# Optimization experiments

Measured on AMD Instinct MI355X. Metric: run time of the kernel, lower is better.

## Reference

```python
import jax, jax.numpy as jnp
import numpy as np

B, S, I, H = 8, 4096, 512, 512


def setup_inputs() -> dict:
    key = jax.random.key(0)
    ks = jax.random.split(key, 5)
    s_ih = 1.0 / np.sqrt(H)
    return {
        "x": jax.random.normal(ks[0], (B, S, I), dtype=jnp.float32),
        "W_ih": jax.random.uniform(ks[1], (H, I), jnp.float32, -s_ih, s_ih),
        "W_hh": jax.random.uniform(ks[2], (H, H), jnp.float32, -s_ih, s_ih),
        "b_ih": jax.random.uniform(ks[3], (H,), jnp.float32, -s_ih, s_ih),
        "b_hh": jax.random.uniform(ks[4], (H,), jnp.float32, -s_ih, s_ih),
    }


def reference(x, W_ih, W_hh, b_ih, b_hh):
    # Precompute input contribution for all timesteps in one batched GEMM:
    # xp[b,s,h] = x[b,s,:] @ W_ih^T + b_ih
    xp = jnp.einsum("bsi,hi->bsh", x, W_ih) + b_ih  # [B,S,H]
    h0 = jnp.zeros((x.shape[0], W_hh.shape[0]), dtype=x.dtype)

    def step(h, xp_t):
        h = jnp.tanh(xp_t + h @ W_hh.T + b_hh)
        return h, h

    # scan over time (sequential recurrence)
    _, outs = jax.lax.scan(step, h0, jnp.swapaxes(xp, 0, 1))  # outs: [S,B,H]
    return jnp.swapaxes(outs, 0, 1)  # [B,S,H]
```

## Files before the change

### kernel.cpp

```cpp
#include <hip/hip_runtime.h>
#include <hip/hip_fp16.h>

#define BB 8
#define SS 4096
#define II 512
#define HH 512

typedef _Float16 h2_t __attribute__((ext_vector_type(2)));

__device__ __forceinline__ unsigned int pack_h2(float a, float b) {
    h2_t p;
    p.x = (_Float16)a;
    p.y = (_Float16)b;
    return __builtin_bit_cast(unsigned int, p);
}

__device__ __forceinline__ float dot2acc(unsigned int hp, unsigned int wp, float acc) {
#if __has_builtin(__builtin_amdgcn_fdot2)
    return __builtin_amdgcn_fdot2(__builtin_bit_cast(h2_t, hp),
                                  __builtin_bit_cast(h2_t, wp), acc, false);
#else
    h2_t h = __builtin_bit_cast(h2_t, hp);
    h2_t w = __builtin_bit_cast(h2_t, wp);
    acc = fmaf((float)h.x, (float)w.x, acc);
    acc = fmaf((float)h.y, (float)w.y, acc);
    return acc;
#endif
}

__device__ __forceinline__ float tanh_fast(float x) {
    float ax = fabsf(x);
    float t  = exp2f(-2.8853900817779268f * ax);
    float r  = (1.0f - t) * __builtin_amdgcn_rcpf(1.0f + t);
    return copysignf(r, x);
}

#define P1_TM 64
#define P1_TN 64
#define P1_TK 16
#define P1_LDP 68

__global__ __launch_bounds__(256) void xp_gemm(const float* __restrict__ x,
                                               const float* __restrict__ wih,
                                               const float* __restrict__ bih,
                                               float* __restrict__ out) {
    __shared__ float As[P1_TK][P1_LDP];
    __shared__ float Bs[P1_TK][P1_LDP];
    const int tid = threadIdx.x;
    const int n0  = blockIdx.x * P1_TN;
    const int m0  = blockIdx.y * P1_TM;
    const int row = tid >> 2;
    const int f4  = tid & 3;
    const int ty  = tid >> 4;
    const int tx  = tid & 15;

    float acc[4][4];
#pragma unroll
    for (int r = 0; r < 4; ++r)
#pragma unroll
        for (int c = 0; c < 4; ++c) acc[r][c] = 0.0f;

    const float* xa = x   + (size_t)(m0 + row) * II + f4 * 4;
    const float* wb = wih + (size_t)(n0 + row) * II + f4 * 4;

    for (int kb = 0; kb < II; kb += P1_TK) {
        float4 av = *(const float4*)(xa + kb);
        float4 bv = *(const float4*)(wb + kb);
        __syncthreads();
        As[f4 * 4 + 0][row] = av.x; As[f4 * 4 + 1][row] = av.y;
        As[f4 * 4 + 2][row] = av.z; As[f4 * 4 + 3][row] = av.w;
        Bs[f4 * 4 + 0][row] = bv.x; Bs[f4 * 4 + 1][row] = bv.y;
        Bs[f4 * 4 + 2][row] = bv.z; Bs[f4 * 4 + 3][row] = bv.w;
        __syncthreads();
#pragma unroll
        for (int kk = 0; kk < P1_TK; ++kk) {
            const float* a4 = &As[kk][ty * 4];
            const float* b4 = &Bs[kk][tx * 4];
#pragma unroll
            for (int r = 0; r < 4; ++r)
#pragma unroll
                for (int c = 0; c < 4; ++c)
                    acc[r][c] = fmaf(a4[r], b4[c], acc[r][c]);
        }
    }

    const float4 bias = *(const float4*)&bih[n0 + tx * 4];
#pragma unroll
    for (int r = 0; r < 4; ++r) {
        float4 v;
        v.x = acc[r][0] + bias.x;
        v.y = acc[r][1] + bias.y;
        v.z = acc[r][2] + bias.z;
        v.w = acc[r][3] + bias.w;
        *(float4*)(out + (size_t)(m0 + ty * 4 + r) * HH + n0 + tx * 4) = v;
    }
}

#define KREG 384
#define NREG (KREG / 2)
#define KLDS (HH - KREG)
#define W2P  66
#define LDS_DW (256 + HH * W2P)

__global__ __launch_bounds__(512, 2) void rnn_scan(const float* __restrict__ whh,
                                                   const float* __restrict__ bhh,
                                                   float* __restrict__ io) {
    extern __shared__ unsigned int lds[];
    unsigned int* hbuf = lds;
    unsigned int* w2   = lds + 256;

    const int b = blockIdx.x;
    const int j = threadIdx.x;

    unsigned int wreg[NREG];
    const float* wrow = whh + (size_t)j * HH;
#pragma unroll
    for (int q4 = 0; q4 < KREG / 4; ++q4) {
        float4 f = *(const float4*)(wrow + q4 * 4);
        wreg[2 * q4 + 0] = pack_h2(f.x, f.y);
        wreg[2 * q4 + 1] = pack_h2(f.z, f.w);
    }

    for (int idx = j; idx < HH * (KLDS / 2); idx += 512) {
        int jj = idx >> 6;
        int q  = idx & 63;
        const float* p = whh + (size_t)jj * HH + KREG + 2 * q;
        w2[jj * W2P + q] = pack_h2(p[0], p[1]);
    }
    if (j < 256) hbuf[j] = 0u;
    const float bj = bhh[j];
    __syncthreads();

    float* iob = io + (size_t)b * SS * HH;
    float xp_cur = iob[j];
    const unsigned int* wl = w2 + j * W2P;

#pragma unroll 1
    for (int t = 0; t < SS; ++t) {
        const int tn = (t + 1 < SS) ? t + 1 : t;
        float xp_next = iob[(size_t)tn * HH + j];

        float a0 = xp_cur + bj, a1 = 0.0f, a2 = 0.0f, a3 = 0.0f;

#pragma unroll
        for (int c = 0; c < NREG / 4; ++c) {
            uint4 hv = *(const uint4*)&hbuf[4 * c];
            a0 = dot2acc(hv.x, wreg[4 * c + 0], a0);
            a1 = dot2acc(hv.y, wreg[4 * c + 1], a1);
            a2 = dot2acc(hv.z, wreg[4 * c + 2], a2);
            a3 = dot2acc(hv.w, wreg[4 * c + 3], a3);
        }
#pragma unroll
        for (int c = 0; c < (KLDS / 2) / 4; ++c) {
            uint4 hv = *(const uint4*)&hbuf[NREG + 4 * c];
            uint2 wa = *(const uint2*)&wl[4 * c];
            uint2 wc = *(const uint2*)&wl[4 * c + 2];
            a0 = dot2acc(hv.x, wa.x, a0);
            a1 = dot2acc(hv.y, wa.y, a1);
            a2 = dot2acc(hv.z, wc.x, a2);
            a3 = dot2acc(hv.w, wc.y, a3);
        }

        float hnew = tanh_fast((a0 + a1) + (a2 + a3));
        iob[(size_t)t * HH + j] = hnew;
        __syncthreads();
        ((_Float16*)hbuf)[j] = (_Float16)hnew;
        __syncthreads();
        xp_cur = xp_next;
    }
}

extern "C" void kernel_launch(void* const* d_in, const int* in_sizes, int n_in,
                              void* d_out, int out_size, void* d_ws, size_t ws_size,
                              hipStream_t stream) {
    const float* x   = (const float*)d_in[0];
    const float* wih = (const float*)d_in[1];
    const float* whh = (const float*)d_in[2];
    const float* bih = (const float*)d_in[3];
    const float* bhh = (const float*)d_in[4];
    float* out = (float*)d_out;

    dim3 g1(HH / P1_TN, (BB * SS) / P1_TM);
    xp_gemm<<<g1, 256, 0, stream>>>(x, wih, bih, out);

    static_assert(LDS_DW * 4 <= 163840, "LDS over 160 KiB");
    hipFuncSetAttribute((const void*)rnn_scan,
                        hipFuncAttributeMaxDynamicSharedMemorySize, LDS_DW * 4);
    rnn_scan<<<dim3(BB), dim3(512), LDS_DW * 4, stream>>>(whh, bhh, out);
}
```

Baseline: 6.765 ms.

## Run RNN recurrence with MFMA across two cooperating blocks exchanging hidden state

Replaces the per-batch scan (one block per batch, dot2 per thread) with two blocks that each own half of the hidden columns for all 8 batches. Each block keeps its W_hh slice in registers as f16 and uses 16x16x32 MFMA on the batch-padded hidden state. After each step the blocks swap their new hidden halves through a global double-buffered mailbox, synchronised by an atomic flag spin. This removes the redundant per-batch weight traffic and turns the matvec into matrix cores, at the cost of a cross-CU global handshake every timestep and wasted MFMA rows from padding 8 batches to 16.

```diff
diff --git a/kernel.cpp b/kernel.cpp
--- a/kernel.cpp
+++ b/kernel.cpp
@@ -6,27 +6,8 @@
 #define II 512
 #define HH 512
 
-typedef _Float16 h2_t __attribute__((ext_vector_type(2)));
-
-__device__ __forceinline__ unsigned int pack_h2(float a, float b) {
-    h2_t p;
-    p.x = (_Float16)a;
-    p.y = (_Float16)b;
-    return __builtin_bit_cast(unsigned int, p);
-}
-
-__device__ __forceinline__ float dot2acc(unsigned int hp, unsigned int wp, float acc) {
-#if __has_builtin(__builtin_amdgcn_fdot2)
-    return __builtin_amdgcn_fdot2(__builtin_bit_cast(h2_t, hp),
-                                  __builtin_bit_cast(h2_t, wp), acc, false);
-#else
-    h2_t h = __builtin_bit_cast(h2_t, hp);
-    h2_t w = __builtin_bit_cast(h2_t, wp);
-    acc = fmaf((float)h.x, (float)w.x, acc);
-    acc = fmaf((float)h.y, (float)w.y, acc);
-    return acc;
-#endif
-}
+typedef _Float16 f16x8 __attribute__((ext_vector_type(8)));
+typedef float f32x4 __attribute__((ext_vector_type(4)));
 
 __device__ __forceinline__ float tanh_fast(float x) {
     float ax = fabsf(x);
@@ -96,77 +77,119 @@
     }
 }
 
-#define KREG 384
-#define NREG (KREG / 2)
-#define KLDS (HH - KREG)
-#define W2P  66
-#define LDS_DW (256 + HH * W2P)
-
-__global__ __launch_bounds__(512, 2) void rnn_scan(const float* __restrict__ whh,
-                                                   const float* __restrict__ bhh,
-                                                   float* __restrict__ io) {
-    extern __shared__ unsigned int lds[];
-    unsigned int* hbuf = lds;
-    unsigned int* w2   = lds + 256;
-
-    const int b = blockIdx.x;
-    const int j = threadIdx.x;
-
-    unsigned int wreg[NREG];
-    const float* wrow = whh + (size_t)j * HH;
-#pragma unroll
-    for (int q4 = 0; q4 < KREG / 4; ++q4) {
-        float4 f = *(const float4*)(wrow + q4 * 4);
-        wreg[2 * q4 + 0] = pack_h2(f.x, f.y);
-        wreg[2 * q4 + 1] = pack_h2(f.z, f.w);
-    }
-
-    for (int idx = j; idx < HH * (KLDS / 2); idx += 512) {
-        int jj = idx >> 6;
-        int q  = idx & 63;
-        const float* p = whh + (size_t)jj * HH + KREG + 2 * q;
-        w2[jj * W2P + q] = pack_h2(p[0], p[1]);
-    }
-    if (j < 256) hbuf[j] = 0u;
-    const float bj = bhh[j];
-    __syncthreads();
-
-    float* iob = io + (size_t)b * SS * HH;
-    float xp_cur = iob[j];
-    const unsigned int* wl = w2 + j * W2P;
-
-#pragma unroll 1
+__global__ __launch_bounds__(256, 1) void rnn_scan2(
+    const float* __restrict__ whh, const float* __restrict__ bhh,
+    float* __restrict__ io, unsigned int* __restrict__ flags,
+    uint4* __restrict__ mail ) {
+    const int bid = blockIdx.x;
+    if (bid != 0 && bid != 8) return;
+    const int p   = bid ? 1 : 0;
+    const int tid = threadIdx.x;
+    const int w   = tid >> 6;
+    const int l   = tid & 63;
+    const int l15 = l & 15;
+    const int lh  = l >> 4;
+
+    __shared__ _Float16 hh[8][264];
+
+    int ncol[4];
+#pragma unroll
+    for (int i = 0; i < 4; ++i) ncol[i] = p * 256 + (w * 4 + i) * 16 + l15;
+
+    f16x8 wf[4][16];
+#pragma unroll
+    for (int i = 0; i < 4; ++i) {
+        const float* wr = whh + (size_t)ncol[i] * HH;
+#pragma unroll
+        for (int kb = 0; kb < 16; ++kb) {
+            const int k0 = kb * 32 + lh * 8;
+            float4 x0 = *(const float4*)(wr + k0);
+            float4 x1 = *(const float4*)(wr + k0 + 4);
+            f16x8 f;
+            f[0] = (_Float16)x0.x; f[1] = (_Float16)x0.y;
+            f[2] = (_Float16)x0.z; f[3] = (_Float16)x0.w;
+            f[4] = (_Float16)x1.x; f[5] = (_Float16)x1.y;
+            f[6] = (_Float16)x1.z; f[7] = (_Float16)x1.w;
+            wf[i][kb] = f;
+        }
+    }
+    float bv[4];
+#pragma unroll
+    for (int i = 0; i < 4; ++i) bv[i] = bhh[ncol[i]];
+
     for (int t = 0; t < SS; ++t) {
-        const int tn = (t + 1 < SS) ? t + 1 : t;
-        float xp_next = iob[(size_t)tn * HH + j];
-
-        float a0 = xp_cur + bj, a1 = 0.0f, a2 = 0.0f, a3 = 0.0f;
-
-#pragma unroll
-        for (int c = 0; c < NREG / 4; ++c) {
-            uint4 hv = *(const uint4*)&hbuf[4 * c];
-            a0 = dot2acc(hv.x, wreg[4 * c + 0], a0);
-            a1 = dot2acc(hv.y, wreg[4 * c + 1], a1);
-            a2 = dot2acc(hv.z, wreg[4 * c + 2], a2);
-            a3 = dot2acc(hv.w, wreg[4 * c + 3], a3);
-        }
-#pragma unroll
-        for (int c = 0; c < (KLDS / 2) / 4; ++c) {
-            uint4 hv = *(const uint4*)&hbuf[NREG + 4 * c];
-            uint2 wa = *(const uint2*)&wl[4 * c];
-            uint2 wc = *(const uint2*)&wl[4 * c + 2];
-            a0 = dot2acc(hv.x, wa.x, a0);
-            a1 = dot2acc(hv.y, wa.y, a1);
-            a2 = dot2acc(hv.z, wc.x, a2);
-            a3 = dot2acc(hv.w, wc.y, a3);
-        }
-
-        float hnew = tanh_fast((a0 + a1) + (a2 + a3));
-        iob[(size_t)t * HH + j] = hnew;
-        __syncthreads();
-        ((_Float16*)hbuf)[j] = (_Float16)hnew;
-        __syncthreads();
-        xp_cur = xp_next;
+        float xq[4][4];
+        if (lh < 2) {
+#pragma unroll
+            for (int r = 0; r < 4; ++r) {
+                const int m = lh * 4 + r;
+                const float* row = io + ((size_t)m * SS + t) * HH;
+#pragma unroll
+                for (int i = 0; i < 4; ++i) xq[r][i] = row[ncol[i]];
+            }
+        }
+
+        f32x4 acc[4];
+#pragma unroll
+        for (int i = 0; i < 4; ++i) acc[i] = (f32x4){0.f, 0.f, 0.f, 0.f};
+
+        if (t > 0) {
+            if (tid == 0) {
+                while (__hip_atomic_load(flags + (1 - p) * 64, __ATOMIC_RELAXED,
+                                         __HIP_MEMORY_SCOPE_AGENT) < (unsigned)t)
+                    __builtin_amdgcn_s_sleep(1);
+            }
+            __syncthreads();
+            __threadfence();
+
+            const uint4* mb = mail + (size_t)((t - 1) & 1) * 1024;
+            f16x8 af[16];
+#pragma unroll
+            for (int kb = 0; kb < 16; ++kb) {
+                uint4 u = mb[kb * 64 + l];
+                af[kb] = __builtin_bit_cast(f16x8, u);
+            }
+#pragma unroll
+            for (int kb = 0; kb < 16; ++kb)
+#pragma unroll
+                for (int i = 0; i < 4; ++i)
+                    acc[i] = __builtin_amdgcn_mfma_f32_16x16x32_f16(
+                        af[kb], wf[i][kb], acc[i], 0, 0, 0);
+        }
+
+        if (lh < 2) {
+#pragma unroll
+            for (int r = 0; r < 4; ++r) {
+                const int m = lh * 4 + r;
+                float* row = io + ((size_t)m * SS + t) * HH;
+#pragma unroll
+                for (int i = 0; i < 4; ++i) {
+                    float v = tanh_fast(acc[i][r] + xq[r][i] + bv[i]);
+                    row[ncol[i]] = v;
+                    hh[m][(w * 4 + i) * 16 + l15] = (_Float16)v;
+                }
+            }
+        }
+        __syncthreads();
+
+#pragma unroll
+        for (int e2 = 0; e2 < 2; ++e2) {
+            const int e   = tid * 2 + e2;
+            const int kbl = e >> 6;
+            const int ll  = e & 63;
+            const int m   = ll & 15;
+            uint4 v = make_uint4(0u, 0u, 0u, 0u);
+            if (m < 8) {
+                const int nloc = kbl * 32 + (ll >> 4) * 8;
+                v = *(const uint4*)&hh[m][nloc];
+            }
+            mail[(size_t)(t & 1) * 1024 + (size_t)(p * 8 + kbl) * 64 + ll] = v;
+        }
+        __threadfence();
+        __syncthreads();
+        if (tid == 0)
+            __hip_atomic_store(flags + p * 64, (unsigned)(t + 1),
+                               __ATOMIC_RELAXED, __HIP_MEMORY_SCOPE_AGENT);
     }
 }
 
@@ -180,11 +203,13 @@
     const float* bhh = (const float*)d_in[4];
     float* out = (float*)d_out;
 
+    unsigned int* flags = (unsigned int*)d_ws;
+    uint4* mail = (uint4*)((char*)d_ws + 4096);
+
+    hipMemsetAsync(d_ws, 0, 4096, stream);
+
     dim3 g1(HH / P1_TN, (BB * SS) / P1_TM);
     xp_gemm<<<g1, 256, 0, stream>>>(x, wih, bih, out);
 
-    static_assert(LDS_DW * 4 <= 163840, "LDS over 160 KiB");
-    hipFuncSetAttribute((const void*)rnn_scan,
-                        hipFuncAttributeMaxDynamicSharedMemorySize, LDS_DW * 4);
-    rnn_scan<<<dim3(BB), dim3(512), LDS_DW * 4, stream>>>(whh, bhh, out);
-}
+    rnn_scan2<<<dim3(16), dim3(256), 0, stream>>>(whh, bhh, out, flags, mail);
+}
```

New measurement: 24.16 ms. 257% more time.
